# Performance work log

Measured on AMD Instinct MI355X. Metric: run time of the kernel, lower is better.

The kernel has to match this reference:

```python
import jax, jax.numpy as jnp
import numpy as np

N = 100000
E = 1600000
F_IN = 602
NHID = 128
N_CLS = 41


def setup_inputs() -> dict:
    key = jax.random.key(0)
    k1, k2, k3, k4 = jax.random.split(key, 4)
    x = jax.random.normal(k1, (N, F_IN), dtype=jnp.float32)
    edge_index = jax.random.randint(k2, (2, E), 0, N, dtype=jnp.int64)
    # Glorot-style scaled weights
    W1 = jax.random.normal(k3, (F_IN, NHID), dtype=jnp.float32) * (1.0 / np.sqrt(F_IN))
    b1 = jnp.zeros((NHID,), dtype=jnp.float32)
    W2 = jax.random.normal(k4, (NHID, N_CLS), dtype=jnp.float32) * (1.0 / np.sqrt(NHID))
    b2 = jnp.zeros((N_CLS,), dtype=jnp.float32)
    return {"x": x, "edge_index": edge_index, "W1": W1, "b1": b1, "W2": W2, "b2": b2}


def reference(x, edge_index, W1, b1, W2, b2):
    n = x.shape[0]
    loop = jnp.arange(n, dtype=edge_index.dtype)
    # PyG GCNConv: add self-loops, symmetric normalization D^-1/2 (A+I) D^-1/2
    src = jnp.concatenate([edge_index[0], loop])  # [E+N]
    dst = jnp.concatenate([edge_index[1], loop])  # [E+N]
    ones = jnp.ones(src.shape[0], dtype=x.dtype)
    deg = jax.ops.segment_sum(ones, dst, num_segments=n)  # in-degree incl self-loop
    dinv = jnp.where(deg > 0, jax.lax.rsqrt(deg), 0.0)
    norm = dinv[src] * dinv[dst]  # [E+N]

    def conv(h, W, b):
        h = h @ W  # transform first (smaller feature dim for gather)
        msg = h[src] * norm[:, None]  # gather + scale
        return jax.ops.segment_sum(msg, dst, num_segments=n) + b  # scatter-add

    h = jax.nn.relu(conv(x, W1, b1))
    # dropout is identity in eval mode
    out = conv(h, W2, b2)
    return jax.nn.log_softmax(out, axis=1)
```

## Files before the change

kernel.cpp:

```cpp
#include <hip/hip_runtime.h>
#include <math.h>

#define GK 602
#define GH 128
#define GC 41
#define GCP 48
#define KPAD 608
#define NKT 19
#define W1FN (NKT * 4096)

typedef __bf16 bf16x8 __attribute__((ext_vector_type(8)));
typedef float f32x16 __attribute__((ext_vector_type(16)));

__device__ __forceinline__ unsigned short f2bf(float f) {
    __bf16 b = (__bf16)f;
    return __builtin_bit_cast(unsigned short, b);
}
__device__ __forceinline__ float bf2f(unsigned short u) {
    return __uint_as_float((unsigned int)u << 16);
}
__device__ __forceinline__ float bflo(unsigned int u) { return __uint_as_float(u << 16); }
__device__ __forceinline__ float bfhi(unsigned int u) { return __uint_as_float(u & 0xffff0000u); }

__device__ __forceinline__ void gl_lds16(const float* g, float* l) {
    __builtin_amdgcn_global_load_lds((const __attribute__((address_space(1))) void*)g,
                                     (__attribute__((address_space(3))) void*)l, 16, 0, 0);
}
__device__ __forceinline__ void gl_lds4(const float* g, float* l) {
    __builtin_amdgcn_global_load_lds((const __attribute__((address_space(1))) void*)g,
                                     (__attribute__((address_space(3))) void*)l, 4, 0, 0);
}


__global__ void k_pre(const float* __restrict__ W1, unsigned short* __restrict__ W1F,
                      const int* __restrict__ dst, int* __restrict__ counts,
                      int E, int nbPrep) {
    if ((int)blockIdx.x < nbPrep) {
        int i = blockIdx.x * 256 + threadIdx.x;
        if (i >= W1FN) return;
        int kt = i >> 12;
        int r  = i & 4095;
        int nt = r >> 10;
        int r2 = r & 1023;
        int bs = r2 >> 9;
        int r3 = r2 & 511;
        int ln = r3 >> 3;
        int j  = r3 & 7;
        int col = 32 * nt + (ln & 31);
        int k   = 32 * kt + 16 * bs + 8 * (ln >> 5) + j;
        float v = (k < GK) ? W1[(size_t)k * GH + col] : 0.f;
        W1F[i] = f2bf(v);
    } else {
        int g = (blockIdx.x - nbPrep) * 256 + threadIdx.x;
        int base = g * 4;
        if (((E & 3) == 0) && (base + 3 < E)) {
            int4 d4 = *(const int4*)(dst + base);
            atomicAdd(&counts[d4.x], 1);
            atomicAdd(&counts[d4.y], 1);
            atomicAdd(&counts[d4.z], 1);
            atomicAdd(&counts[d4.w], 1);
        } else {
#pragma unroll
            for (int j2 = 0; j2 < 4; ++j2) {
                int e = base + j2;
                if (e < E) atomicAdd(&counts[dst[e]], 1);
            }
        }
    }
}

__global__ void k_scan_a(const int* __restrict__ counts, int* __restrict__ row_ptr,
                         int* __restrict__ bsum, int n) {
    __shared__ int wsum[4];
    int t = threadIdx.x;
    int lane = t & 63;
    int wv = t >> 6;
    int base = blockIdx.x * 1024 + t * 4;
    int v[4];
    int s = 0;
#pragma unroll
    for (int j = 0; j < 4; ++j) {
        int idx = base + j;
        v[j] = (idx < n) ? counts[idx] : 0;
        s += v[j];
    }
    int incl = s;
#pragma unroll
    for (int o = 1; o < 64; o <<= 1) {
        int x = __shfl_up(incl, o);
        if (lane >= o) incl += x;
    }
    if (lane == 63) wsum[wv] = incl;
    __syncthreads();
    int woff = 0;
#pragma unroll
    for (int i = 0; i < 3; ++i) woff += (i < wv) ? wsum[i] : 0;
    if (t == 255) bsum[blockIdx.x] = woff + incl;
    int off = woff + incl - s;
#pragma unroll
    for (int j = 0; j < 4; ++j) {
        int idx = base + j;
        if (idx < n) row_ptr[idx] = off;
        off += v[j];
    }
}

__global__ void k_scan_b(int* __restrict__ bsum, int nb) {
    __shared__ int sh[256];
    int t = threadIdx.x;
    int v = (t < nb) ? bsum[t] : 0;
    sh[t] = v;
    __syncthreads();
    for (int o = 1; o < 256; o <<= 1) {
        int x = (t >= o) ? sh[t - o] : 0;
        __syncthreads();
        sh[t] += x;
        __syncthreads();
    }
    if (t < nb) bsum[t] = sh[t] - v;
}

__global__ void k_scan_c(int* __restrict__ row_ptr, const int* __restrict__ bsum,
                         const int* __restrict__ counts, float* __restrict__ dinv,
                         int* __restrict__ cursor, int n, int E) {
    int i = blockIdx.x * 256 + threadIdx.x;
    if (i < n) {
        int rp = row_ptr[i] + bsum[i >> 10];
        row_ptr[i] = rp;
        cursor[i] = rp;
        dinv[i] = rsqrtf((float)(counts[i] + 1));
    }
    if (i == 0) row_ptr[n] = E;
}


#define SLABF (32 * GK)

__global__ __launch_bounds__(256, 2) void k_gemm1_fill(
        const float* __restrict__ X, const unsigned short* __restrict__ W1F,
        unsigned short* __restrict__ Y, int M,
        const int* __restrict__ src, const int* __restrict__ dst,
        const float* __restrict__ dinv, int* __restrict__ cursor,
        int2* __restrict__ meta, int E, int nbG) {
    if ((int)blockIdx.x >= nbG) {
        int g = (blockIdx.x - nbG) * 256 + threadIdx.x;
        int base = g * 4;
        if (((E & 3) == 0) && (base + 3 < E)) {
            int4 s4 = *(const int4*)(src + base);
            int4 d4 = *(const int4*)(dst + base);
            int ss[4] = {s4.x, s4.y, s4.z, s4.w};
            int dd[4] = {d4.x, d4.y, d4.z, d4.w};
#pragma unroll
            for (int j = 0; j < 4; ++j) {
                int p = atomicAdd(&cursor[dd[j]], 1);
                float w = dinv[ss[j]] * dinv[dd[j]];
                meta[p] = make_int2(ss[j], __float_as_int(w));
            }
        } else {
#pragma unroll
            for (int j = 0; j < 4; ++j) {
                int e = base + j;
                if (e < E) {
                    int s = src[e];
                    int d = dst[e];
                    int p = atomicAdd(&cursor[d], 1);
                    float w = dinv[s] * dinv[d];
                    meta[p] = make_int2(s, __float_as_int(w));
                }
            }
        }
        return;
    }

    __shared__ float As[SLABF + 16];
    int tid = threadIdx.x;
    int lane = tid & 63;
    int w = tid >> 6;
    int rowBase = blockIdx.x * 32;
    const float* slab = X + (size_t)rowBase * GK;

#pragma unroll
    for (int r = 0; r < 18; ++r) {
        int c = tid + 256 * r;
        gl_lds16(slab + 4 * c, &As[4 * c]);
    }
    if (w < 3) {
        int c = 4608 + (w << 6) + lane;
        gl_lds16(slab + 4 * c, &As[4 * c]);
    } else {
        int f = 19200 + lane;
        gl_lds4(slab + f, &As[f]);
    }
    if (tid < 16) As[SLABF + tid] = 0.f;
    asm volatile("s_waitcnt vmcnt(0)" ::: "memory");
    __syncthreads();

    int arow = lane & 31;
    int kh = 8 * (lane >> 5);
    const float* Ar = &As[arow * GK];
    const unsigned short* Wb = W1F + (size_t)w * 1024 + (size_t)lane * 8;

    f32x16 acc;
#pragma unroll
    for (int i = 0; i < 16; ++i) acc[i] = 0.f;

#pragma unroll
    for (int t = 0; t < NKT; ++t) {
        const unsigned short* Wt = Wb + (size_t)t * 4096;
        bf16x8 b0 = *(const bf16x8*)(Wt);
        bf16x8 b1 = *(const bf16x8*)(Wt + 512);
        const float* a0p = Ar + 32 * t + kh;
        float2 p0 = *(const float2*)(a0p + 0);
        float2 p1 = *(const float2*)(a0p + 2);
        float2 p2 = *(const float2*)(a0p + 4);
        float2 p3 = *(const float2*)(a0p + 6);
        const float* a1p = a0p + 16;
        float2 q0 = *(const float2*)(a1p + 0);
        float2 q1 = *(const float2*)(a1p + 2);
        float2 q2 = *(const float2*)(a1p + 4);
        float2 q3 = *(const float2*)(a1p + 6);
        bf16x8 af0, af1;
        af0[0] = (__bf16)p0.x; af0[1] = (__bf16)p0.y;
        af0[2] = (__bf16)p1.x; af0[3] = (__bf16)p1.y;
        af0[4] = (__bf16)p2.x; af0[5] = (__bf16)p2.y;
        af0[6] = (__bf16)p3.x; af0[7] = (__bf16)p3.y;
        af1[0] = (__bf16)q0.x; af1[1] = (__bf16)q0.y;
        af1[2] = (__bf16)q1.x; af1[3] = (__bf16)q1.y;
        af1[4] = (__bf16)q2.x; af1[5] = (__bf16)q2.y;
        af1[6] = (__bf16)q3.x; af1[7] = (__bf16)q3.y;
        acc = __builtin_amdgcn_mfma_f32_32x32x16_bf16(af0, b0, acc, 0, 0, 0);
        acc = __builtin_amdgcn_mfma_f32_32x32x16_bf16(af1, b1, acc, 0, 0, 0);
    }

    int gcol = 32 * w + (lane & 31);
#pragma unroll
    for (int reg = 0; reg < 16; ++reg) {
        int rrow = (reg & 3) + 8 * (reg >> 2) + 4 * (lane >> 5);
        int grow = rowBase + rrow;
        if (grow < M) Y[(size_t)grow * GH + gcol] = f2bf(acc[reg]);
    }
}


__global__ __launch_bounds__(256) void k_agg1(const unsigned int* __restrict__ H,
                                              unsigned int* __restrict__ O,
                                              const int* __restrict__ row_ptr,
                                              const int2* __restrict__ meta,
                                              const float* __restrict__ dinv,
                                              const float* __restrict__ bias, int n) {
    int wv = threadIdx.x >> 6;
    int lane = threadIdx.x & 63;
    int d = blockIdx.x * 4 + wv;
    if (d >= n) return;
    float dd = dinv[d];
    int beg = row_ptr[d], end = row_ptr[d + 1];
    unsigned int v = H[(size_t)d * 64 + lane];
    float sw = dd * dd;
    float a0 = sw * bflo(v);
    float a1 = sw * bfhi(v);
    int e = beg;
    for (; e + 16 <= end; e += 16) {
        int2 m[16];
        unsigned int u[16];
#pragma unroll
        for (int j = 0; j < 16; ++j) m[j] = meta[e + j];
#pragma unroll
        for (int j = 0; j < 16; ++j) u[j] = H[(size_t)m[j].x * 64 + lane];
#pragma unroll
        for (int j = 0; j < 16; ++j) {
            float wj = __int_as_float(m[j].y);
            a0 = fmaf(wj, bflo(u[j]), a0);
            a1 = fmaf(wj, bfhi(u[j]), a1);
        }
    }
    if (e + 8 <= end) {
        int2 m[8];
        unsigned int u[8];
#pragma unroll
        for (int j = 0; j < 8; ++j) m[j] = meta[e + j];
#pragma unroll
        for (int j = 0; j < 8; ++j) u[j] = H[(size_t)m[j].x * 64 + lane];
#pragma unroll
        for (int j = 0; j < 8; ++j) {
            float wj = __int_as_float(m[j].y);
            a0 = fmaf(wj, bflo(u[j]), a0);
            a1 = fmaf(wj, bfhi(u[j]), a1);
        }
        e += 8;
    }
    if (e + 4 <= end) {
        int2 m[4];
        unsigned int u[4];
#pragma unroll
        for (int j = 0; j < 4; ++j) m[j] = meta[e + j];
#pragma unroll
        for (int j = 0; j < 4; ++j) u[j] = H[(size_t)m[j].x * 64 + lane];
#pragma unroll
        for (int j = 0; j < 4; ++j) {
            float wj = __int_as_float(m[j].y);
            a0 = fmaf(wj, bflo(u[j]), a0);
            a1 = fmaf(wj, bfhi(u[j]), a1);
        }
        e += 4;
    }
    for (; e < end; ++e) {
        int2 m = meta[e];
        unsigned int u = H[(size_t)m.x * 64 + lane];
        float wj = __int_as_float(m.y);
        a0 = fmaf(wj, bflo(u), a0);
        a1 = fmaf(wj, bfhi(u), a1);
    }
    a0 = fmaxf(a0 + bias[2 * lane], 0.f);
    a1 = fmaxf(a1 + bias[2 * lane + 1], 0.f);
    O[(size_t)d * 64 + lane] = (unsigned int)f2bf(a0) | ((unsigned int)f2bf(a1) << 16);
}


__global__ __launch_bounds__(256) void k_gemm2t(const unsigned int* __restrict__ Hb,
                                                const float* __restrict__ W2,
                                                unsigned short* __restrict__ G, int n) {
    __shared__ float ws[128][GCP];
    for (int i = threadIdx.x; i < 128 * GCP; i += 256) {
        int k = i / GCP;
        int c = i - k * GCP;
        ws[k][c] = (c < GC) ? W2[k * GC + c] : 0.f;
    }
    __syncthreads();
    int r0 = blockIdx.x * 512 + threadIdx.x;
    int r1 = r0 + 256;
    bool v0 = r0 < n, v1 = r1 < n;
    float acc0[GCP], acc1[GCP];
#pragma unroll
    for (int c = 0; c < GCP; ++c) { acc0[c] = 0.f; acc1[c] = 0.f; }
    const uint2* h0 = (const uint2*)(Hb + (size_t)(v0 ? r0 : 0) * 64);
    const uint2* h1 = (const uint2*)(Hb + (size_t)(v1 ? r1 : 0) * 64);
    for (int q = 0; q < 32; ++q) {
        uint2 ua = h0[q];
        uint2 ub = h1[q];
        float va[4] = {bflo(ua.x), bfhi(ua.x), bflo(ua.y), bfhi(ua.y)};
        float vb[4] = {bflo(ub.x), bfhi(ub.x), bflo(ub.y), bfhi(ub.y)};
#pragma unroll
        for (int j = 0; j < 4; ++j) {
            int k = 4 * q + j;
#pragma unroll
            for (int cq = 0; cq < GCP / 4; ++cq) {
                float4 wv = *(const float4*)&ws[k][4 * cq];
                acc0[4 * cq + 0] = fmaf(va[j], wv.x, acc0[4 * cq + 0]);
                acc0[4 * cq + 1] = fmaf(va[j], wv.y, acc0[4 * cq + 1]);
                acc0[4 * cq + 2] = fmaf(va[j], wv.z, acc0[4 * cq + 2]);
                acc0[4 * cq + 3] = fmaf(va[j], wv.w, acc0[4 * cq + 3]);
                acc1[4 * cq + 0] = fmaf(vb[j], wv.x, acc1[4 * cq + 0]);
                acc1[4 * cq + 1] = fmaf(vb[j], wv.y, acc1[4 * cq + 1]);
                acc1[4 * cq + 2] = fmaf(vb[j], wv.z, acc1[4 * cq + 2]);
                acc1[4 * cq + 3] = fmaf(vb[j], wv.w, acc1[4 * cq + 3]);
            }
        }
    }
    if (v0) {
#pragma unroll
        for (int c = 0; c < GCP; ++c) G[(size_t)r0 * GCP + c] = f2bf(acc0[c]);
    }
    if (v1) {
#pragma unroll
        for (int c = 0; c < GCP; ++c) G[(size_t)r1 * GCP + c] = f2bf(acc1[c]);
    }
}


__global__ __launch_bounds__(256) void k_agg2(const unsigned short* __restrict__ G,
                                              float* __restrict__ out,
                                              const int* __restrict__ row_ptr,
                                              const int2* __restrict__ meta,
                                              const float* __restrict__ dinv,
                                              const float* __restrict__ b2, int n) {
    int wv = threadIdx.x >> 6;
    int lane = threadIdx.x & 63;
    int gl = (lane < GCP) ? lane : (GCP - 1);
    int d = blockIdx.x * 4 + wv;
    if (d >= n) return;
    float dd = dinv[d];
    int beg = row_ptr[d], end = row_ptr[d + 1];
    float a = dd * dd * bf2f(G[(size_t)d * GCP + gl]);
    int e = beg;
    for (; e + 16 <= end; e += 16) {
        int2 m[16];
        unsigned short u[16];
#pragma unroll
        for (int j = 0; j < 16; ++j) m[j] = meta[e + j];
#pragma unroll
        for (int j = 0; j < 16; ++j) u[j] = G[(size_t)m[j].x * GCP + gl];
#pragma unroll
        for (int j = 0; j < 16; ++j) a = fmaf(__int_as_float(m[j].y), bf2f(u[j]), a);
    }
    if (e + 8 <= end) {
        int2 m[8];
        unsigned short u[8];
#pragma unroll
        for (int j = 0; j < 8; ++j) m[j] = meta[e + j];
#pragma unroll
        for (int j = 0; j < 8; ++j) u[j] = G[(size_t)m[j].x * GCP + gl];
#pragma unroll
        for (int j = 0; j < 8; ++j) a = fmaf(__int_as_float(m[j].y), bf2f(u[j]), a);
        e += 8;
    }
    if (e + 4 <= end) {
        int2 m[4];
        unsigned short u[4];
#pragma unroll
        for (int j = 0; j < 4; ++j) m[j] = meta[e + j];
#pragma unroll
        for (int j = 0; j < 4; ++j) u[j] = G[(size_t)m[j].x * GCP + gl];
#pragma unroll
        for (int j = 0; j < 4; ++j) a = fmaf(__int_as_float(m[j].y), bf2f(u[j]), a);
        e += 4;
    }
    for (; e < end; ++e) {
        int2 m = meta[e];
        a = fmaf(__int_as_float(m.y), bf2f(G[(size_t)m.x * GCP + gl]), a);
    }
    float logit = (lane < GC) ? (a + b2[lane]) : -INFINITY;
    float mx = logit;
#pragma unroll
    for (int off = 32; off; off >>= 1) mx = fmaxf(mx, __shfl_xor(mx, off));
    float ex = (lane < GC) ? __expf(logit - mx) : 0.f;
    float sm = ex;
#pragma unroll
    for (int off = 32; off; off >>= 1) sm += __shfl_xor(sm, off);
    if (lane < GC) out[(size_t)d * GC + lane] = logit - mx - __logf(sm);
}


static inline size_t alignup256(size_t x) { return (x + 255) & ~(size_t)255; }

extern "C" void kernel_launch(void* const* d_in, const int* in_sizes, int n_in,
                              void* d_out, int out_size, void* d_ws, size_t ws_size,
                              hipStream_t stream) {
    const float* x  = (const float*)d_in[0];
    const int*   ei = (const int*)d_in[1];
    const float* W1 = (const float*)d_in[2];
    const float* b1 = (const float*)d_in[3];
    const float* W2 = (const float*)d_in[4];
    const float* b2 = (const float*)d_in[5];
    float* out = (float*)d_out;

    const int n = in_sizes[0] / GK;
    const int E = in_sizes[1] / 2;
    const int* src = ei;
    const int* dst = ei + E;

    char* w = (char*)d_ws;
    char* p;
    p = w; w += alignup256((size_t)n * 4);            float* dinv  = (float*)p;
    p = w; w += alignup256((size_t)n * 4);            int* counts  = (int*)p;
    p = w; w += alignup256((size_t)n * 4);            int* cursor  = (int*)p;
    p = w; w += alignup256((size_t)(n + 1) * 4);      int* row_ptr = (int*)p;
    p = w; w += alignup256(1024 * 4);                 int* bsum    = (int*)p;
    p = w; w += alignup256((size_t)E * 8);            int2* meta   = (int2*)p;
    p = w; w += alignup256((size_t)GH * KPAD * 2);    unsigned short* W1F = (unsigned short*)p;
    p = w; w += alignup256((size_t)n * GH * 2);       unsigned short* bufA = (unsigned short*)p;
    p = w; w += alignup256((size_t)n * GH * 2);       unsigned short* bufB = (unsigned short*)p;
    p = w; w += alignup256((size_t)n * GCP * 2);      unsigned short* G    = (unsigned short*)p;

    hipMemsetAsync(counts, 0, (size_t)n * 4, stream);

    int gN = (n + 255) / 256;
    int nb = (n + 1023) / 1024;
    int nbPrep = (W1FN + 255) / 256;
    int nbHist = (E / 4 + 255) / 256;
    int nbG    = (n + 31) / 32;

    k_pre<<<nbPrep + nbHist, 256, 0, stream>>>(W1, W1F, dst, counts, E, nbPrep);
    k_scan_a<<<nb, 256, 0, stream>>>(counts, row_ptr, bsum, n);
    k_scan_b<<<1, 256, 0, stream>>>(bsum, nb);
    k_scan_c<<<gN, 256, 0, stream>>>(row_ptr, bsum, counts, dinv, cursor, n, E);

    k_gemm1_fill<<<nbG + nbHist, 256, 0, stream>>>(x, W1F, bufA, n,
                                                   src, dst, dinv, cursor, meta, E, nbG);
    k_agg1<<<(n + 3) / 4, 256, 0, stream>>>((const unsigned int*)bufA, (unsigned int*)bufB,
                                            row_ptr, meta, dinv, b1, n);
    k_gemm2t<<<(n + 511) / 512, 256, 0, stream>>>((const unsigned int*)bufB, W2, G, n);
    k_agg2<<<(n + 3) / 4, 256, 0, stream>>>(G, out, row_ptr, meta, dinv, b2, n);
}
```

Measured before the change: 668.5 us.

## Switch GEMM1 to 16-row tiles with 16x16x32 MFMA and reorder fill blocks

```diff
diff --git a/kernel.cpp b/kernel.cpp
--- a/kernel.cpp
+++ b/kernel.cpp
@@ -5,12 +5,11 @@
 #define GH 128
 #define GC 41
 #define GCP 48
-#define KPAD 608
 #define NKT 19
-#define W1FN (NKT * 4096)
+#define W1FN (NKT * 8 * 512)
 
 typedef __bf16 bf16x8 __attribute__((ext_vector_type(8)));
-typedef float f32x16 __attribute__((ext_vector_type(16)));
+typedef float f32x4 __attribute__((ext_vector_type(4)));
 
 __device__ __forceinline__ unsigned short f2bf(float f) {
     __bf16 b = (__bf16)f;
@@ -25,10 +24,6 @@
 __device__ __forceinline__ void gl_lds16(const float* g, float* l) {
     __builtin_amdgcn_global_load_lds((const __attribute__((address_space(1))) void*)g,
                                      (__attribute__((address_space(3))) void*)l, 16, 0, 0);
-}
-__device__ __forceinline__ void gl_lds4(const float* g, float* l) {
-    __builtin_amdgcn_global_load_lds((const __attribute__((address_space(1))) void*)g,
-                                     (__attribute__((address_space(3))) void*)l, 4, 0, 0);
 }
 
 
@@ -38,16 +33,14 @@
     if ((int)blockIdx.x < nbPrep) {
         int i = blockIdx.x * 256 + threadIdx.x;
         if (i >= W1FN) return;
-        int kt = i >> 12;
+        int t  = i >> 12;
         int r  = i & 4095;
-        int nt = r >> 10;
-        int r2 = r & 1023;
-        int bs = r2 >> 9;
-        int r3 = r2 & 511;
-        int ln = r3 >> 3;
-        int j  = r3 & 7;
-        int col = 32 * nt + (ln & 31);
-        int k   = 32 * kt + 16 * bs + 8 * (ln >> 5) + j;
+        int nt = r >> 9;
+        int r2 = r & 511;
+        int ln = r2 >> 3;
+        int j  = r2 & 7;
+        int col = 16 * nt + (ln & 15);
+        int k   = 32 * t + 8 * (ln >> 4) + j;
         float v = (k < GK) ? W1[(size_t)k * GH + col] : 0.f;
         W1F[i] = f2bf(v);
     } else {
@@ -134,16 +127,17 @@
 }
 
 
-#define SLABF (32 * GK)
-
-__global__ __launch_bounds__(256, 2) void k_gemm1_fill(
+#define STAGEF 10240
+
+__global__ __launch_bounds__(256, 4) void k_gemm1_fill(
         const float* __restrict__ X, const unsigned short* __restrict__ W1F,
         unsigned short* __restrict__ Y, int M,
         const int* __restrict__ src, const int* __restrict__ dst,
         const float* __restrict__ dinv, int* __restrict__ cursor,
-        int2* __restrict__ meta, int E, int nbG) {
-    if ((int)blockIdx.x >= nbG) {
-        int g = (blockIdx.x - nbG) * 256 + threadIdx.x;
+        int2* __restrict__ meta, int E, int nbF) {
+    __shared__ float As[STAGEF];
+    if ((int)blockIdx.x < nbF) {
+        int g = blockIdx.x * 256 + threadIdx.x;
         int base = g * 4;
         if (((E & 3) == 0) && (base + 3 < E)) {
             int4 s4 = *(const int4*)(src + base);
@@ -172,72 +166,60 @@
         return;
     }
 
-    __shared__ float As[SLABF + 16];
     int tid = threadIdx.x;
     int lane = tid & 63;
     int w = tid >> 6;
-    int rowBase = blockIdx.x * 32;
+    int rowBase = (blockIdx.x - nbF) * 16;
     const float* slab = X + (size_t)rowBase * GK;
-
-#pragma unroll
-    for (int r = 0; r < 18; ++r) {
+    const float* xlim = X + (size_t)M * GK - 4;
+
+#pragma unroll
+    for (int r = 0; r < 10; ++r) {
         int c = tid + 256 * r;
-        gl_lds16(slab + 4 * c, &As[4 * c]);
-    }
-    if (w < 3) {
-        int c = 4608 + (w << 6) + lane;
-        gl_lds16(slab + 4 * c, &As[4 * c]);
-    } else {
-        int f = 19200 + lane;
-        gl_lds4(slab + f, &As[f]);
-    }
-    if (tid < 16) As[SLABF + tid] = 0.f;
+        const float* s = slab + 4 * c;
+        if (s > xlim) s = xlim;
+        gl_lds16(s, &As[4 * c]);
+    }
     asm volatile("s_waitcnt vmcnt(0)" ::: "memory");
     __syncthreads();
 
-    int arow = lane & 31;
-    int kh = 8 * (lane >> 5);
+    int arow = lane & 15;
+    int kh = 8 * (lane >> 4);
     const float* Ar = &As[arow * GK];
-    const unsigned short* Wb = W1F + (size_t)w * 1024 + (size_t)lane * 8;
-
-    f32x16 acc;
-#pragma unroll
-    for (int i = 0; i < 16; ++i) acc[i] = 0.f;
+    const unsigned short* Wb = W1F + (size_t)lane * 8;
+
+    f32x4 acc0, acc1;
+#pragma unroll
+    for (int i = 0; i < 4; ++i) { acc0[i] = 0.f; acc1[i] = 0.f; }
 
 #pragma unroll
     for (int t = 0; t < NKT; ++t) {
-        const unsigned short* Wt = Wb + (size_t)t * 4096;
-        bf16x8 b0 = *(const bf16x8*)(Wt);
-        bf16x8 b1 = *(const bf16x8*)(Wt + 512);
-        const float* a0p = Ar + 32 * t + kh;
-        float2 p0 = *(const float2*)(a0p + 0);
-        float2 p1 = *(const float2*)(a0p + 2);
-        float2 p2 = *(const float2*)(a0p + 4);
-        float2 p3 = *(const float2*)(a0p + 6);
-        const float* a1p = a0p + 16;
-        float2 q0 = *(const float2*)(a1p + 0);
-        float2 q1 = *(const float2*)(a1p + 2);
-        float2 q2 = *(const float2*)(a1p + 4);
-        float2 q3 = *(const float2*)(a1p + 6);
-        bf16x8 af0, af1;
-        af0[0] = (__bf16)p0.x; af0[1] = (__bf16)p0.y;
-        af0[2] = (__bf16)p1.x; af0[3] = (__bf16)p1.y;
-        af0[4] = (__bf16)p2.x; af0[5] = (__bf16)p2.y;
-        af0[6] = (__bf16)p3.x; af0[7] = (__bf16)p3.y;
-        af1[0] = (__bf16)q0.x; af1[1] = (__bf16)q0.y;
-        af1[2] = (__bf16)q1.x; af1[3] = (__bf16)q1.y;
-        af1[4] = (__bf16)q2.x; af1[5] = (__bf16)q2.y;
-        af1[6] = (__bf16)q3.x; af1[7] = (__bf16)q3.y;
-        acc = __builtin_amdgcn_mfma_f32_32x32x16_bf16(af0, b0, acc, 0, 0, 0);
-        acc = __builtin_amdgcn_mfma_f32_32x32x16_bf16(af1, b1, acc, 0, 0, 0);
-    }
-
-    int gcol = 32 * w + (lane & 31);
-#pragma unroll
-    for (int reg = 0; reg < 16; ++reg) {
-        int rrow = (reg & 3) + 8 * (reg >> 2) + 4 * (lane >> 5);
-        int grow = rowBase + rrow;
-        if (grow < M) Y[(size_t)grow * GH + gcol] = f2bf(acc[reg]);
+        const float* ap = Ar + 32 * t + kh;
+        float2 p0 = *(const float2*)(ap + 0);
+        float2 p1 = *(const float2*)(ap + 2);
+        float2 p2 = *(const float2*)(ap + 4);
+        float2 p3 = *(const float2*)(ap + 6);
+        bf16x8 af;
+        af[0] = (__bf16)p0.x; af[1] = (__bf16)p0.y;
+        af[2] = (__bf16)p1.x; af[3] = (__bf16)p1.y;
+        af[4] = (__bf16)p2.x; af[5] = (__bf16)p2.y;
+        af[6] = (__bf16)p3.x; af[7] = (__bf16)p3.y;
+        bf16x8 b0 = *(const bf16x8*)(Wb + (size_t)(8 * t + 2 * w) * 512);
+        bf16x8 b1 = *(const bf16x8*)(Wb + (size_t)(8 * t + 2 * w + 1) * 512);
+        acc0 = __builtin_amdgcn_mfma_f32_16x16x32_bf16(af, b0, acc0, 0, 0, 0);
+        acc1 = __builtin_amdgcn_mfma_f32_16x16x32_bf16(af, b1, acc1, 0, 0, 0);
+    }
+
+    int rbase = rowBase + 4 * (lane >> 4);
+    int c0 = 16 * (2 * w) + (lane & 15);
+    int c1 = 16 * (2 * w + 1) + (lane & 15);
+#pragma unroll
+    for (int reg = 0; reg < 4; ++reg) {
+        int grow = rbase + reg;
+        if (grow < M) {
+            Y[(size_t)grow * GH + c0] = f2bf(acc0[reg]);
+            Y[(size_t)grow * GH + c1] = f2bf(acc1[reg]);
+        }
     }
 }
 
@@ -456,7 +438,7 @@
     p = w; w += alignup256((size_t)(n + 1) * 4);      int* row_ptr = (int*)p;
     p = w; w += alignup256(1024 * 4);                 int* bsum    = (int*)p;
     p = w; w += alignup256((size_t)E * 8);            int2* meta   = (int2*)p;
-    p = w; w += alignup256((size_t)GH * KPAD * 2);    unsigned short* W1F = (unsigned short*)p;
+    p = w; w += alignup256((size_t)W1FN * 2);         unsigned short* W1F = (unsigned short*)p;
     p = w; w += alignup256((size_t)n * GH * 2);       unsigned short* bufA = (unsigned short*)p;
     p = w; w += alignup256((size_t)n * GH * 2);       unsigned short* bufB = (unsigned short*)p;
     p = w; w += alignup256((size_t)n * GCP * 2);      unsigned short* G    = (unsigned short*)p;
@@ -467,15 +449,15 @@
     int nb = (n + 1023) / 1024;
     int nbPrep = (W1FN + 255) / 256;
     int nbHist = (E / 4 + 255) / 256;
-    int nbG    = (n + 31) / 32;
+    int nbG    = (n + 15) / 16;
 
     k_pre<<<nbPrep + nbHist, 256, 0, stream>>>(W1, W1F, dst, counts, E, nbPrep);
     k_scan_a<<<nb, 256, 0, stream>>>(counts, row_ptr, bsum, n);
     k_scan_b<<<1, 256, 0, stream>>>(bsum, nb);
     k_scan_c<<<gN, 256, 0, stream>>>(row_ptr, bsum, counts, dinv, cursor, n, E);
 
-    k_gemm1_fill<<<nbG + nbHist, 256, 0, stream>>>(x, W1F, bufA, n,
-                                                   src, dst, dinv, cursor, meta, E, nbG);
+    k_gemm1_fill<<<nbHist + nbG, 256, 0, stream>>>(x, W1F, bufA, n,
+                                                   src, dst, dinv, cursor, meta, E, nbHist);
     k_agg1<<<(n + 3) / 4, 256, 0, stream>>>((const unsigned int*)bufA, (unsigned int*)bufB,
                                             row_ptr, meta, dinv, b1, n);
     k_gemm2t<<<(n + 511) / 512, 256, 0, stream>>>((const unsigned int*)bufB, W2, G, n);
```

Result: no change. 668.6 us (+0.0%).
